# Performance work log

Measured on AMD Instinct MI355X. Metric: run time of the kernel, lower is better.

The kernel has to match this reference:

```python
import jax, jax.numpy as jnp
import numpy as np
from jax import lax

B, C, H, W = 8, 384, 64, 64


def cos_map(N):
    # ortho DCT-II basis: weight[n, x] = cos(n*(x+0.5)*pi/N) * sqrt(2/N), row 0 /= sqrt(2)
    wx = (jnp.arange(N, dtype=jnp.float32) + 0.5) / N
    wn = jnp.arange(N, dtype=jnp.float32)[:, None]
    w = jnp.cos(wn * wx[None, :] * jnp.pi) * np.sqrt(2.0 / N).astype(np.float32)
    return w.at[0, :].multiply(np.float32(1.0 / np.sqrt(2.0)))


def setup_inputs() -> dict:
    key = jax.random.key(0)
    ks = jax.random.split(key, 8)
    s = 0.05
    return {
        "x": jax.random.normal(ks[0], (B, C, H, W), jnp.float32),
        "freq_embed": jax.random.normal(ks[1], (H, W, C), jnp.float32),
        "dw_w": jax.random.normal(ks[2], (C, 1, 3, 3), jnp.float32) * s,
        "dw_b": jnp.zeros((C,), jnp.float32),
        "lin_w": jax.random.normal(ks[3], (2 * C, C), jnp.float32) * s,
        "lin_b": jnp.zeros((2 * C,), jnp.float32),
        "tok_w": jax.random.normal(ks[4], (C, C), jnp.float32) * s,
        "tok_b": jnp.zeros((C,), jnp.float32),
        "c": jnp.ones((1,), jnp.float32),
        "alpha": jnp.ones((1,), jnp.float32) * 0.1,
        "ln_g": jnp.ones((C,), jnp.float32),
        "ln_b": jnp.zeros((C,), jnp.float32),
        "out_w": jax.random.normal(ks[5], (C, C), jnp.float32) * s,
        "out_b": jnp.zeros((C,), jnp.float32),
    }


def reference(x, freq_embed, dw_w, dw_b, lin_w, lin_b, tok_w, tok_b, c, alpha, ln_g, ln_b, out_w, out_b):
    Bc, Cc, Hc, Wc = x.shape
    # depthwise 3x3 conv
    x = lax.conv_general_dilated(x, dw_w, (1, 1), 'SAME',
                                 feature_group_count=Cc,
                                 dimension_numbers=('NCHW', 'OIHW', 'NCHW'))
    x = x + dw_b[None, :, None, None]
    # linear to 2C (channels-last), split into signal x and gate z
    xz = jnp.einsum('bchw,dc->bhwd', x, lin_w) + lin_b
    xs, z = xz[..., :Cc], xz[..., Cc:]          # [B,H,W,C]
    xs = jnp.transpose(xs, (0, 3, 1, 2))        # [B,C,H,W]
    # 2D ortho DCT-II: D = Wh @ x @ Ww^T
    Wh, Ww = cos_map(Hc), cos_map(Wc)
    Xd = jnp.einsum('nh,bchw,kw->bcnk', Wh, xs, Ww)
    # learned frequency gating: t = ReLU(Linear(freq_embed)), per (H,W,C)
    t = jax.nn.relu(jnp.einsum('hwc,dc->hwd', freq_embed, tok_w) + tok_b)
    ct = jnp.transpose(jnp.cos(c * t), (2, 0, 1))[None]        # [1,C,H,W]
    st = jnp.transpose(jnp.sin(c * t), (2, 0, 1))[None] / c[0]
    # x_u0 == x_v0 == Xd in the original (dct2d applied twice to same x)
    final = ct * Xd + st * (Xd + 0.5 * alpha[0] * Xd)
    # 2D inverse DCT: x = Wh^T @ D @ Ww
    xi = jnp.einsum('nh,bcnk,kw->bchw', Wh, final, Ww)
    # LayerNorm over channels, gate with SiLU(z), output linear
    y = jnp.transpose(xi, (0, 2, 3, 1))          # [B,H,W,C]
    mu = jnp.mean(y, axis=-1, keepdims=True)
    var = jnp.mean((y - mu) ** 2, axis=-1, keepdims=True)
    y = (y - mu) * lax.rsqrt(var + 1e-5) * ln_g + ln_b
    y = y * jax.nn.silu(z)
    y = jnp.einsum('bhwc,dc->bhwd', y, out_w) + out_b
    return jnp.transpose(y, (0, 3, 1, 2))        # [B,C,H,W]
```

## Files before the change

kernel.cpp:

```cpp
#include <hip/hip_runtime.h>

typedef _Float16 h2 __attribute__((ext_vector_type(2)));
typedef _Float16 h4 __attribute__((ext_vector_type(4)));
typedef _Float16 h8 __attribute__((ext_vector_type(8)));
typedef float    f4 __attribute__((ext_vector_type(4)));

#define MFMA32(a,b,c) __builtin_amdgcn_mfma_f32_16x16x32_f16((a),(b),(c),0,0,0)
#define MFMA16(a,b,c) __builtin_amdgcn_mfma_f32_16x16x16f16((a),(b),(c),0,0,0)

#define B_N 8
#define C_N 384
#define P_N 4096
#define PI_F 3.14159265358979323846f

__device__ __forceinline__ h4 to_h4(f4 v) {
  h4 r; r[0]=(_Float16)v[0]; r[1]=(_Float16)v[1]; r[2]=(_Float16)v[2]; r[3]=(_Float16)v[3];
  return r;
}

__device__ __forceinline__ void gl_lds16(const _Float16* g, _Float16* l) {
  __builtin_amdgcn_global_load_lds(
      (const __attribute__((address_space(1))) void*)g,
      (__attribute__((address_space(3))) void*)l, 16, 0, 0);
}

__device__ __forceinline__ void gemm_step(
    const _Float16* __restrict__ ga, const _Float16* __restrict__ gb,
    int kcn, bool pref,
    _Float16* laC, _Float16* lbC, _Float16* laN, _Float16* lbN,
    f4 (&acc)[4][4]) {
  int t = threadIdx.x, lane = t & 63, wave = t >> 6;
  int quad = lane >> 4, l15 = lane & 15;
  int wm = wave >> 1, wn = wave & 1;
  int s_row = lane >> 2;
  if (pref) {
    #pragma unroll
    for (int s = 0; s < 2; s++) {
      int seg = wave * 2 + s;
      int row = seg * 16 + s_row;
      gl_lds16(ga + (size_t)row*384 + kcn, &laN[seg*512 + lane*8]);
      gl_lds16(gb + (size_t)row*384 + kcn, &lbN[seg*512 + lane*8]);
    }
    asm volatile("s_waitcnt vmcnt(4)" ::: "memory");
  } else {
    asm volatile("s_waitcnt vmcnt(0)" ::: "memory");
  }
  __builtin_amdgcn_s_barrier();
  asm volatile("" ::: "memory");
  h8 af[4], bf[4];
  int sq = (quad ^ (l15 & 3)) * 8;
  #pragma unroll
  for (int i = 0; i < 4; i++) {
    af[i] = *(const h8*)&laC[(wm*64 + i*16 + l15)*32 + sq];
    bf[i] = *(const h8*)&lbC[(wn*64 + i*16 + l15)*32 + sq];
  }
  asm volatile("s_waitcnt lgkmcnt(0)" ::: "memory");
  __builtin_amdgcn_s_barrier();
  asm volatile("" ::: "memory");
  #pragma unroll
  for (int i = 0; i < 4; i++)
  #pragma unroll
  for (int j = 0; j < 4; j++)
    acc[i][j] = MFMA32(af[i], bf[j], acc[i][j]);
}

__global__ __launch_bounds__(256) void k_setup(
    const float* __restrict__ lin_w, const float* __restrict__ tok_w,
    const float* __restrict__ out_w, _Float16* __restrict__ lwh,
    _Float16* __restrict__ twh, _Float16* __restrict__ owh,
    _Float16* __restrict__ wmg, _Float16* __restrict__ wmtg) {
  int t = blockIdx.x * 256 + threadIdx.x;
  if (t < 768*384) lwh[t] = (_Float16)lin_w[t];
  if (t < 384*384) { twh[t] = (_Float16)tok_w[t]; owh[t] = (_Float16)out_w[t]; }
  if (t < 4096) {
    int n = t >> 6, h = t & 63;
    float v = cosf((float)n * ((float)h + 0.5f) * (PI_F / 64.0f)) * 0.1767766952966369f;
    if (n == 0) v *= 0.7071067811865476f;
    wmg[n*64 + h]  = (_Float16)v;
    wmtg[h*64 + n] = (_Float16)v;
  }
}

__global__ __launch_bounds__(256) void k_dwconv(
    const float* __restrict__ x, const float* __restrict__ dww,
    const float* __restrict__ dwb, _Float16* __restrict__ xdw) {
  int blk = blockIdx.x;
  int h = blk & 63;
  int rest = blk >> 6;
  int cgi = rest % 6;
  int b = rest / 6;
  int c0 = cgi * 64;
  int t = threadIdx.x;
  __shared__ float wsm[576];
  __shared__ float bsm[64];
  __shared__ _Float16 buf[64 * 68];
  for (int i = t; i < 576; i += 256) wsm[i] = dww[c0*9 + i];
  if (t < 64) bsm[t] = dwb[c0 + t];
  __syncthreads();
  int lane = t & 63;
  int wslot = lane & 15, w4 = wslot * 4;
  int cs = t >> 4;
  bool wlo = (wslot == 0), whi = (wslot == 15);
  int lm = (lane - 1) & 63, lp = (lane + 1) & 63;
  const float* xb = x + (size_t)b * C_N * P_N;
  float pr[4][4];
  #pragma unroll
  for (int q = 0; q < 4; q++) {
    int lc = cs * 4 + q;
    const float* xc = xb + (size_t)(c0 + lc) * P_N + h * 64 + w4;
    f4 mid = *(const f4*)xc;
    f4 top = {}, bot = {};
    if (h > 0)  top = *(const f4*)(xc - 64);
    if (h < 63) bot = *(const f4*)(xc + 64);
    float tL = __shfl(top[3], lm, 64), tR = __shfl(top[0], lp, 64);
    float mL = __shfl(mid[3], lm, 64), mR = __shfl(mid[0], lp, 64);
    float bL = __shfl(bot[3], lm, 64), bR = __shfl(bot[0], lp, 64);
    if (wlo) { tL = 0.f; mL = 0.f; bL = 0.f; }
    if (whi) { tR = 0.f; mR = 0.f; bR = 0.f; }
    float k0=wsm[lc*9+0],k1=wsm[lc*9+1],k2=wsm[lc*9+2];
    float k3=wsm[lc*9+3],k4=wsm[lc*9+4],k5=wsm[lc*9+5];
    float k6=wsm[lc*9+6],k7=wsm[lc*9+7],k8=wsm[lc*9+8];
    float bias = bsm[lc];
    #pragma unroll
    for (int e = 0; e < 4; e++) {
      float tl = (e > 0) ? top[e-1] : tL;
      float tr = (e < 3) ? top[e+1] : tR;
      float ml = (e > 0) ? mid[e-1] : mL;
      float mr = (e < 3) ? mid[e+1] : mR;
      float bl = (e > 0) ? bot[e-1] : bL;
      float br = (e < 3) ? bot[e+1] : bR;
      float acc = bias;
      acc += k0*tl + k1*top[e] + k2*tr;
      acc += k3*ml + k4*mid[e] + k5*mr;
      acc += k6*bl + k7*bot[e] + k8*br;
      pr[q][e] = acc;
    }
  }
  #pragma unroll
  for (int e = 0; e < 4; e++) {
    h4 hv;
    #pragma unroll
    for (int q = 0; q < 4; q++) hv[q] = (_Float16)pr[q][e];
    *(h4*)&buf[(w4 + e) * 68 + cs * 4] = hv;
  }
  __syncthreads();
  _Float16* op = xdw + ((size_t)b*P_N + h*64) * C_N + c0;
  #pragma unroll
  for (int i = 0; i < 4; i++) {
    int flat = (t + 256*i) * 4;
    int pix = flat >> 6, cl = flat & 63;
    *(h4*)&op[(size_t)pix*C_N + cl] = *(const h4*)&buf[pix*68 + cl];
  }
}

__global__ __launch_bounds__(256) void k_gate(
    const float* __restrict__ fe, const _Float16* __restrict__ twh,
    const float* __restrict__ tkb, const float* __restrict__ cc,
    const float* __restrict__ aa, _Float16* __restrict__ g) {
  int pt = blockIdx.x & 63, dt = blockIdx.x >> 6;
  int p0 = pt*64, d0 = dt*64;
  int t = threadIdx.x, lane = t & 63, wave = t >> 6;
  int quad = lane >> 4, l15 = lane & 15;
  int wm_ = wave >> 1, wn = wave & 1;
  __shared__ _Float16 la[64*40], lb[64*40];
  int srow = t >> 2, scg = (t & 3) * 8;
  f4 acc[2][2] = {};
  for (int kc = 0; kc < 384; kc += 32) {
    const float* src = fe + (size_t)(p0 + srow)*384 + kc + scg;
    f4 v0 = *(const f4*)src;
    f4 v1 = *(const f4*)(src + 4);
    h8 hv;
    hv[0]=(_Float16)v0[0]; hv[1]=(_Float16)v0[1]; hv[2]=(_Float16)v0[2]; hv[3]=(_Float16)v0[3];
    hv[4]=(_Float16)v1[0]; hv[5]=(_Float16)v1[1]; hv[6]=(_Float16)v1[2]; hv[7]=(_Float16)v1[3];
    *(h8*)&la[srow*40 + scg] = hv;
    *(h8*)&lb[srow*40 + scg] = *(const h8*)&twh[(size_t)(d0 + srow)*384 + kc + scg];
    __syncthreads();
    h8 a0 = *(const h8*)&la[(wm_*32 + l15)*40 + quad*8];
    h8 a1 = *(const h8*)&la[(wm_*32 + 16 + l15)*40 + quad*8];
    h8 b0 = *(const h8*)&lb[(wn*32 + l15)*40 + quad*8];
    h8 b1 = *(const h8*)&lb[(wn*32 + 16 + l15)*40 + quad*8];
    acc[0][0] = MFMA32(a0, b0, acc[0][0]);
    acc[0][1] = MFMA32(a0, b1, acc[0][1]);
    acc[1][0] = MFMA32(a1, b0, acc[1][0]);
    acc[1][1] = MFMA32(a1, b1, acc[1][1]);
    __syncthreads();
  }
  float c0 = cc[0];
  float s1 = (1.0f + 0.5f*aa[0]) / c0;
  #pragma unroll
  for (int i = 0; i < 2; i++)
  #pragma unroll
  for (int j = 0; j < 2; j++) {
    int d  = d0 + wn*32 + j*16 + l15;
    int pl = wm_*32 + i*16 + quad*4;
    float bias = tkb[d];
    h4 hv;
    #pragma unroll
    for (int r = 0; r < 4; r++) {
      float tv = fmaxf(acc[i][j][r] + bias, 0.0f);
      hv[r] = (_Float16)(__cosf(c0*tv) + s1*__sinf(c0*tv));
    }
    *(h4*)&g[(size_t)d*P_N + p0 + pl] = hv;
  }
}

__global__ __launch_bounds__(256) void k_gemm1(
    const _Float16* __restrict__ xdw, const _Float16* __restrict__ lwh,
    const float* __restrict__ lnb, _Float16* __restrict__ xs,
    _Float16* __restrict__ zs) {
  int pt = blockIdx.x & 31;
  int rest = blockIdx.x >> 5;
  int dt = rest % 6, b = rest / 6;
  int p0 = pt * 128, d0 = dt * 128;
  int t = threadIdx.x, lane = t & 63, wave = t >> 6;
  int quad = lane >> 4, l15 = lane & 15;
  int wm = wave >> 1, wn = wave & 1;
  __shared__ _Float16 la0[128 * 32], lb0[128 * 32];
  __shared__ _Float16 la1[128 * 32], lb1[128 * 32];
  int s_row = lane >> 2;
  int scol2 = (((lane & 3) ^ (s_row & 3)) * 8);
  const _Float16* ga = xdw + ((size_t)b*P_N + p0) * 384 + scol2;
  const _Float16* gb = lwh + (size_t)d0 * 384 + scol2;
  f4 acc[4][4] = {};
  #pragma unroll
  for (int s = 0; s < 2; s++) {
    int seg = wave * 2 + s;
    int row = seg * 16 + s_row;
    gl_lds16(ga + (size_t)row*384, &la0[seg*512 + lane*8]);
    gl_lds16(gb + (size_t)row*384, &lb0[seg*512 + lane*8]);
  }
  #pragma unroll
  for (int kt = 0; kt < 6; kt++) {
    int kc = kt * 64;
    gemm_step(ga, gb, kc + 32,  true,            la0, lb0, la1, lb1, acc);
    gemm_step(ga, gb, kc + 64,  (kc + 64 < 384), la1, lb1, la0, lb0, acc);
  }
  bool isz = (d0 >= 384);
  #pragma unroll
  for (int j = 0; j < 4; j++) {
    int d = d0 + wn*64 + j*16 + l15;
    float bias = lnb[d];
    _Float16* dst = isz ? (zs + ((size_t)b*C_N + (d-384)) * P_N)
                        : (xs + ((size_t)b*C_N + d) * P_N);
    #pragma unroll
    for (int i = 0; i < 4; i++) {
      int p = p0 + wm*64 + i*16 + quad*4;
      h4 hv;
      if (isz) {
        #pragma unroll
        for (int r = 0; r < 4; r++) {
          float v = acc[i][j][r] + bias;
          v = v / (1.0f + __expf(-v));
          hv[r] = (_Float16)v;
        }
      } else {
        #pragma unroll
        for (int r = 0; r < 4; r++) hv[r] = (_Float16)(acc[i][j][r] + bias);
      }
      *(h4*)&dst[p] = hv;
    }
  }
}

__global__ __launch_bounds__(256) void k_dct(
    const _Float16* __restrict__ xs, const _Float16* __restrict__ g,
    const _Float16* __restrict__ wmg, const _Float16* __restrict__ wmtg,
    _Float16* __restrict__ xi) {
  int b = blockIdx.x / 96, cg = blockIdx.x % 96;
  int c0 = cg * 4;
  int t = threadIdx.x, wave = t >> 6, lane = t & 63;
  int quad = lane >> 4, l15 = lane & 15;
  __shared__ _Float16 wm_s[64*72];
  __shared__ _Float16 wmt_s[64*72];
  __shared__ _Float16 pb[4][64*72];
  for (int i = t; i < 512; i += 256) {
    int row = i >> 3, col = (i & 7) * 8;
    *(h8*)&wm_s[row*72 + col]  = *(const h8*)&wmg[row*64 + col];
    *(h8*)&wmt_s[row*72 + col] = *(const h8*)&wmtg[row*64 + col];
  }
  const _Float16* xsb = xs + ((size_t)b*C_N + c0) * P_N;
  for (int i = t; i < 2048; i += 256) {
    int pl = i >> 9, idx = i & 511;
    int p = idx * 8, hh = p >> 6, ww = p & 63;
    *(h8*)&pb[pl][hh*72 + ww] = *(const h8*)&xsb[(size_t)pl*P_N + p];
  }
  __syncthreads();
  h8 aS[4][2], bW[4][2];
  #pragma unroll
  for (int I = 0; I < 4; I++)
  #pragma unroll
  for (int kk = 0; kk < 2; kk++) {
    aS[I][kk] = *(const h8*)&pb[wave][(I*16 + l15)*72 + kk*32 + quad*8];
    bW[I][kk] = *(const h8*)&wm_s[(I*16 + l15)*72 + kk*32 + quad*8];
  }
  h4 t1h[4][4];
  #pragma unroll
  for (int I = 0; I < 4; I++)
  #pragma unroll
  for (int J = 0; J < 4; J++) {
    f4 a = {};
    a = MFMA32(aS[I][0], bW[J][0], a);
    a = MFMA32(aS[I][1], bW[J][1], a);
    t1h[I][J] = to_h4(a);
  }
  __syncthreads();
  const _Float16* gb = g + (size_t)c0 * P_N;
  for (int i = t; i < 2048; i += 256) {
    int pl = i >> 9, idx = i & 511;
    int p = idx * 8, hh = p >> 6, ww = p & 63;
    *(h8*)&pb[pl][hh*72 + ww] = *(const h8*)&gb[(size_t)pl*P_N + p];
  }
  __syncthreads();
  f4 t2[4][4] = {};
  #pragma unroll
  for (int I = 0; I < 4; I++)
  #pragma unroll
  for (int K4 = 0; K4 < 4; K4++) {
    h4 af = *(const h4*)&wm_s[(I*16 + l15)*72 + K4*16 + quad*4];
    #pragma unroll
    for (int J = 0; J < 4; J++) t2[I][J] = MFMA16(af, t1h[K4][J], t2[I][J]);
  }
  h4 fh[4][4];
  #pragma unroll
  for (int I = 0; I < 4; I++)
  #pragma unroll
  for (int J = 0; J < 4; J++) {
    int n0 = I*16 + quad*4, k = J*16 + l15;
    h4 r;
    #pragma unroll
    for (int rr = 0; rr < 4; rr++) {
      float gv = (float)pb[wave][(n0+rr)*72 + k];
      r[rr] = (_Float16)(t2[I][J][rr] * gv);
    }
    fh[I][J] = r;
  }
  f4 t3[4][4] = {};
  #pragma unroll
  for (int J = 0; J < 4; J++)
  #pragma unroll
  for (int K4 = 0; K4 < 4; K4++) {
    h4 bf = *(const h4*)&wmt_s[(J*16 + l15)*72 + K4*16 + quad*4];
    #pragma unroll
    for (int I = 0; I < 4; I++) t3[I][J] = MFMA16(fh[K4][I], bf, t3[I][J]);
  }
  h4 t3h[4][4];
  #pragma unroll
  for (int I = 0; I < 4; I++)
  #pragma unroll
  for (int J = 0; J < 4; J++) t3h[I][J] = to_h4(t3[I][J]);
  f4 t4[4][4] = {};
  #pragma unroll
  for (int I = 0; I < 4; I++)
  #pragma unroll
  for (int K4 = 0; K4 < 4; K4++) {
    h4 af = *(const h4*)&wmt_s[(I*16 + l15)*72 + K4*16 + quad*4];
    #pragma unroll
    for (int J = 0; J < 4; J++) t4[I][J] = MFMA16(af, t3h[K4][J], t4[I][J]);
  }
  #pragma unroll
  for (int I = 0; I < 4; I++)
  #pragma unroll
  for (int J = 0; J < 4; J++) {
    int w0 = I*16 + quad*4, hq = J*16 + l15;
    *(h4*)&pb[wave][hq*72 + w0] = to_h4(t4[I][J]);
  }
  __syncthreads();
  _Float16* xib = xi + ((size_t)b*C_N + c0) * P_N;
  for (int i = t; i < 2048; i += 256) {
    int pl = i >> 9, idx = i & 511;
    int p = idx * 8, hh = p >> 6, ww = p & 63;
    *(h8*)&xib[(size_t)pl*P_N + p] = *(const h8*)&pb[pl][hh*72 + ww];
  }
}

__global__ __launch_bounds__(256) void k_ubuild(
    const _Float16* __restrict__ xi, const _Float16* __restrict__ zs,
    const float* __restrict__ lng, const float* __restrict__ lnbv,
    _Float16* __restrict__ u) {
  int b = blockIdx.x >> 6, pt = blockIdx.x & 63;
  int p0 = pt * 64;
  int t = threadIdx.x;
  __shared__ _Float16 ut[64 * 392];
  __shared__ float red[4][64], red2[4][64];
  __shared__ float muL[64], rsL[64];
  const _Float16* xib = xi + (size_t)b * C_N * P_N;
  #pragma unroll
  for (int i = 0; i < 3; i++) {
    int id = t + 256 * i;
    int px0 = (id & 7) * 8;
    int c4 = (id >> 3) * 4;
    h8 v[4];
    #pragma unroll
    for (int q = 0; q < 4; q++)
      v[q] = *(const h8*)&xib[(size_t)(c4 + q) * P_N + p0 + px0];
    #pragma unroll
    for (int e = 0; e < 8; e++) {
      h4 w;
      #pragma unroll
      for (int q = 0; q < 4; q++) w[q] = v[q][e];
      *(h4*)&ut[(px0 + e) * 392 + c4] = w;
    }
  }
  __syncthreads();
  int px = t & 63, seg = t >> 6;
  float s = 0.f, ss = 0.f;
  #pragma unroll
  for (int j = 0; j < 12; j++) {
    h8 v = *(const h8*)&ut[px * 392 + seg * 96 + j * 8];
    #pragma unroll
    for (int e = 0; e < 8; e++) { float f = (float)v[e]; s += f; ss += f * f; }
  }
  red[seg][px] = s; red2[seg][px] = ss;
  __syncthreads();
  if (t < 64) {
    float st  = red[0][t] + red[1][t] + red[2][t] + red[3][t];
    float sst = red2[0][t] + red2[1][t] + red2[2][t] + red2[3][t];
    float m = st * (1.f/384.f);
    float var = sst * (1.f/384.f) - m * m;
    muL[t] = m; rsL[t] = rsqrtf(var + 1e-5f);
  }
  __syncthreads();
  const _Float16* zb = zs + (size_t)b * C_N * P_N;
  #pragma unroll
  for (int i = 0; i < 3; i++) {
    int id = t + 256 * i;
    int px0 = (id & 7) * 8;
    int c4 = (id >> 3) * 4;
    f4 g4 = *(const f4*)&lng[c4];
    f4 b4 = *(const f4*)&lnbv[c4];
    h8 z[4];
    #pragma unroll
    for (int q = 0; q < 4; q++)
      z[q] = *(const h8*)&zb[(size_t)(c4 + q) * P_N + p0 + px0];
    #pragma unroll
    for (int e = 0; e < 8; e++) {
      int p = px0 + e;
      h4 y = *(const h4*)&ut[p * 392 + c4];
      float mu = muL[p], rs = rsL[p];
      #pragma unroll
      for (int q = 0; q < 4; q++) {
        float f = ((float)y[q] - mu) * rs * g4[q] + b4[q];
        y[q] = (_Float16)(f * (float)z[q][e]);
      }
      *(h4*)&ut[p * 392 + c4] = y;
    }
  }
  __syncthreads();
  _Float16* ub = u + ((size_t)b * P_N + p0) * C_N;
  #pragma unroll
  for (int i = 0; i < 12; i++) {
    int idx = t + 256 * i;
    int row = idx / 48, ch = idx % 48;
    *(h8*)&ub[(size_t)row * C_N + ch * 8] = *(const h8*)&ut[row * 392 + ch * 8];
  }
}

__global__ __launch_bounds__(256) void k_gemm2(
    const _Float16* __restrict__ u, const _Float16* __restrict__ owh,
    const float* __restrict__ ob, float* __restrict__ out) {
  int pt = blockIdx.x & 31;
  int rest = blockIdx.x >> 5;
  int dt = rest % 3, b = rest / 3;
  int p0 = pt * 128, d0 = dt * 128;
  int t = threadIdx.x, lane = t & 63, wave = t >> 6;
  int quad = lane >> 4, l15 = lane & 15;
  int wm = wave >> 1, wn = wave & 1;
  __shared__ _Float16 la0[128 * 32], lb0[128 * 32];
  __shared__ _Float16 la1[128 * 32], lb1[128 * 32];
  int s_row = lane >> 2;
  int scol2 = (((lane & 3) ^ (s_row & 3)) * 8);
  const _Float16* ga = u   + ((size_t)b*P_N + p0) * 384 + scol2;
  const _Float16* gb = owh + (size_t)d0 * 384 + scol2;
  f4 acc[4][4] = {};
  #pragma unroll
  for (int s = 0; s < 2; s++) {
    int seg = wave * 2 + s;
    int row = seg * 16 + s_row;
    gl_lds16(ga + (size_t)row*384, &la0[seg*512 + lane*8]);
    gl_lds16(gb + (size_t)row*384, &lb0[seg*512 + lane*8]);
  }
  #pragma unroll
  for (int kt = 0; kt < 6; kt++) {
    int kc = kt * 64;
    gemm_step(ga, gb, kc + 32,  true,            la0, lb0, la1, lb1, acc);
    gemm_step(ga, gb, kc + 64,  (kc + 64 < 384), la1, lb1, la0, lb0, acc);
  }
  #pragma unroll
  for (int j = 0; j < 4; j++) {
    int d = d0 + wn*64 + j*16 + l15;
    float bias = ob[d];
    #pragma unroll
    for (int i = 0; i < 4; i++) {
      int p = p0 + wm*64 + i*16 + quad*4;
      f4 v;
      #pragma unroll
      for (int r = 0; r < 4; r++) v[r] = acc[i][j][r] + bias;
      *(f4*)&out[((size_t)b*C_N + d)*P_N + p] = v;
    }
  }
}

extern "C" void kernel_launch(void* const* d_in, const int* in_sizes, int n_in,
                              void* d_out, int out_size, void* d_ws, size_t ws_size,
                              hipStream_t stream) {
  (void)in_sizes; (void)n_in; (void)out_size; (void)ws_size;
  const float* x    = (const float*)d_in[0];
  const float* fe   = (const float*)d_in[1];
  const float* dww  = (const float*)d_in[2];
  const float* dwb  = (const float*)d_in[3];
  const float* linw = (const float*)d_in[4];
  const float* linb = (const float*)d_in[5];
  const float* tokw = (const float*)d_in[6];
  const float* tokb = (const float*)d_in[7];
  const float* cc   = (const float*)d_in[8];
  const float* aa   = (const float*)d_in[9];
  const float* lng  = (const float*)d_in[10];
  const float* lnbv = (const float*)d_in[11];
  const float* outw = (const float*)d_in[12];
  const float* outb = (const float*)d_in[13];
  float* out = (float*)d_out;

  char* ws = (char*)d_ws;
  size_t off = 0;
  auto alloc = [&](size_t bytes) -> void* {
    void* p = ws + off;
    off += (bytes + 255) & ~(size_t)255;
    return p;
  };
  _Float16* lwh  = (_Float16*)alloc((size_t)768*384*2);
  _Float16* twh  = (_Float16*)alloc((size_t)384*384*2);
  _Float16* owh  = (_Float16*)alloc((size_t)384*384*2);
  _Float16* wmg  = (_Float16*)alloc((size_t)64*64*2);
  _Float16* wmtg = (_Float16*)alloc((size_t)64*64*2);
  _Float16* xdw  = (_Float16*)alloc((size_t)B_N*P_N*C_N*2);
  _Float16* xs   = (_Float16*)alloc((size_t)B_N*C_N*P_N*2);
  _Float16* zs   = (_Float16*)alloc((size_t)B_N*C_N*P_N*2);
  _Float16* gg   = (_Float16*)alloc((size_t)C_N*P_N*2);
  _Float16* xi   = xdw;
  _Float16* uu   = xs;

  k_setup<<<1152, 256, 0, stream>>>(linw, tokw, outw, lwh, twh, owh, wmg, wmtg);
  k_dwconv<<<3072, 256, 0, stream>>>(x, dww, dwb, xdw);
  k_gate<<<384, 256, 0, stream>>>(fe, twh, tokb, cc, aa, gg);
  k_gemm1<<<1536, 256, 0, stream>>>(xdw, lwh, linb, xs, zs);
  k_dct<<<768, 256, 0, stream>>>(xs, gg, wmg, wmtg, xi);
  k_ubuild<<<512, 256, 0, stream>>>(xi, zs, lng, lnbv, uu);
  k_gemm2<<<768, 256, 0, stream>>>(uu, owh, outb, out);
}
```

Baseline: 234.7 us.

## Process four rows per dwconv block with rolling row reuse; transpose gate tile in LDS

The depthwise conv kernel now handles four consecutive rows per block and keeps the previous and current input rows in registers. Each input row is loaded about once instead of three times, and the grid shrinks fourfold. Separately, the DCT kernel now stores the gate tile transposed in LDS, so the gate multiply can read four contiguous halves per lane instead of four strided scalar loads. The cost is more registers and a larger LDS buffer in dwconv, plus fewer blocks to spread across the GPU.

```diff
diff --git a/kernel.cpp b/kernel.cpp
--- a/kernel.cpp
+++ b/kernel.cpp
@@ -85,15 +85,16 @@
     const float* __restrict__ x, const float* __restrict__ dww,
     const float* __restrict__ dwb, _Float16* __restrict__ xdw) {
   int blk = blockIdx.x;
-  int h = blk & 63;
-  int rest = blk >> 6;
+  int hs = blk & 15;
+  int rest = blk >> 4;
   int cgi = rest % 6;
   int b = rest / 6;
   int c0 = cgi * 64;
+  int h0 = hs * 4;
   int t = threadIdx.x;
   __shared__ float wsm[576];
   __shared__ float bsm[64];
-  __shared__ _Float16 buf[64 * 68];
+  __shared__ _Float16 buf[4][64 * 68];
   for (int i = t; i < 576; i += 256) wsm[i] = dww[c0*9 + i];
   if (t < 64) bsm[t] = dwb[c0 + t];
   __syncthreads();
@@ -102,54 +103,70 @@
   int cs = t >> 4;
   bool wlo = (wslot == 0), whi = (wslot == 15);
   int lm = (lane - 1) & 63, lp = (lane + 1) & 63;
-  const float* xb = x + (size_t)b * C_N * P_N;
-  float pr[4][4];
+  const float* xb = x + (size_t)b * C_N * P_N + w4;
+  f4 prev[4], cur[4];
+  float pL[4], pR[4], cL[4], cR[4];
   #pragma unroll
   for (int q = 0; q < 4; q++) {
-    int lc = cs * 4 + q;
-    const float* xc = xb + (size_t)(c0 + lc) * P_N + h * 64 + w4;
-    f4 mid = *(const f4*)xc;
-    f4 top = {}, bot = {};
-    if (h > 0)  top = *(const f4*)(xc - 64);
-    if (h < 63) bot = *(const f4*)(xc + 64);
-    float tL = __shfl(top[3], lm, 64), tR = __shfl(top[0], lp, 64);
-    float mL = __shfl(mid[3], lm, 64), mR = __shfl(mid[0], lp, 64);
-    float bL = __shfl(bot[3], lm, 64), bR = __shfl(bot[0], lp, 64);
-    if (wlo) { tL = 0.f; mL = 0.f; bL = 0.f; }
-    if (whi) { tR = 0.f; mR = 0.f; bR = 0.f; }
-    float k0=wsm[lc*9+0],k1=wsm[lc*9+1],k2=wsm[lc*9+2];
-    float k3=wsm[lc*9+3],k4=wsm[lc*9+4],k5=wsm[lc*9+5];
-    float k6=wsm[lc*9+6],k7=wsm[lc*9+7],k8=wsm[lc*9+8];
-    float bias = bsm[lc];
+    const float* xc = xb + (size_t)(c0 + cs*4 + q) * P_N;
+    prev[q] = (h0 > 0) ? *(const f4*)(xc + (h0-1)*64) : f4{0.f,0.f,0.f,0.f};
+    cur[q]  = *(const f4*)(xc + h0*64);
+    pL[q] = __shfl(prev[q][3], lm, 64); pR[q] = __shfl(prev[q][0], lp, 64);
+    cL[q] = __shfl(cur[q][3],  lm, 64); cR[q] = __shfl(cur[q][0],  lp, 64);
+    if (wlo) { pL[q] = 0.f; cL[q] = 0.f; }
+    if (whi) { pR[q] = 0.f; cR[q] = 0.f; }
+  }
+  #pragma unroll
+  for (int r = 0; r < 4; r++) {
+    int h = h0 + r;
+    float o[4][4];
+    #pragma unroll
+    for (int q = 0; q < 4; q++) {
+      int lc = cs*4 + q;
+      const float* xc = xb + (size_t)(c0 + lc) * P_N;
+      f4 nxt = (h < 63) ? *(const f4*)(xc + (h+1)*64) : f4{0.f,0.f,0.f,0.f};
+      float nL = __shfl(nxt[3], lm, 64), nR = __shfl(nxt[0], lp, 64);
+      if (wlo) nL = 0.f;
+      if (whi) nR = 0.f;
+      float k0=wsm[lc*9+0],k1=wsm[lc*9+1],k2=wsm[lc*9+2];
+      float k3=wsm[lc*9+3],k4=wsm[lc*9+4],k5=wsm[lc*9+5];
+      float k6=wsm[lc*9+6],k7=wsm[lc*9+7],k8=wsm[lc*9+8];
+      float bias = bsm[lc];
+      #pragma unroll
+      for (int e = 0; e < 4; e++) {
+        float tl = (e > 0) ? prev[q][e-1] : pL[q];
+        float tr = (e < 3) ? prev[q][e+1] : pR[q];
+        float ml = (e > 0) ? cur[q][e-1]  : cL[q];
+        float mr = (e < 3) ? cur[q][e+1]  : cR[q];
+        float bl = (e > 0) ? nxt[e-1]     : nL;
+        float br = (e < 3) ? nxt[e+1]     : nR;
+        float acc = bias;
+        acc += k0*tl + k1*prev[q][e] + k2*tr;
+        acc += k3*ml + k4*cur[q][e]  + k5*mr;
+        acc += k6*bl + k7*nxt[e]     + k8*br;
+        o[q][e] = acc;
+      }
+      prev[q] = cur[q]; pL[q] = cL[q]; pR[q] = cR[q];
+      cur[q] = nxt;     cL[q] = nL;    cR[q] = nR;
+    }
     #pragma unroll
     for (int e = 0; e < 4; e++) {
-      float tl = (e > 0) ? top[e-1] : tL;
-      float tr = (e < 3) ? top[e+1] : tR;
-      float ml = (e > 0) ? mid[e-1] : mL;
-      float mr = (e < 3) ? mid[e+1] : mR;
-      float bl = (e > 0) ? bot[e-1] : bL;
-      float br = (e < 3) ? bot[e+1] : bR;
-      float acc = bias;
-      acc += k0*tl + k1*top[e] + k2*tr;
-      acc += k3*ml + k4*mid[e] + k5*mr;
-      acc += k6*bl + k7*bot[e] + k8*br;
-      pr[q][e] = acc;
-    }
-  }
-  #pragma unroll
-  for (int e = 0; e < 4; e++) {
-    h4 hv;
-    #pragma unroll
-    for (int q = 0; q < 4; q++) hv[q] = (_Float16)pr[q][e];
-    *(h4*)&buf[(w4 + e) * 68 + cs * 4] = hv;
-  }
-  __syncthreads();
-  _Float16* op = xdw + ((size_t)b*P_N + h*64) * C_N + c0;
-  #pragma unroll
-  for (int i = 0; i < 4; i++) {
-    int flat = (t + 256*i) * 4;
-    int pix = flat >> 6, cl = flat & 63;
-    *(h4*)&op[(size_t)pix*C_N + cl] = *(const h4*)&buf[pix*68 + cl];
+      h4 hv;
+      #pragma unroll
+      for (int q = 0; q < 4; q++) hv[q] = (_Float16)o[q][e];
+      *(h4*)&buf[r][(w4 + e) * 68 + cs * 4] = hv;
+    }
+  }
+  __syncthreads();
+  #pragma unroll
+  for (int r = 0; r < 4; r++) {
+    _Float16* op = xdw + ((size_t)b*P_N + (h0 + r)*64) * C_N + c0;
+    #pragma unroll
+    for (int i = 0; i < 4; i++) {
+      int flat = (t + 256*i) * 4;
+      int pix = flat >> 6, cl = flat & 63;
+      *(h4*)&op[(size_t)pix*C_N + cl] = *(const h4*)&buf[r][pix*68 + cl];
+    }
   }
 }
 
@@ -305,10 +322,24 @@
   }
   __syncthreads();
   const _Float16* gb = g + (size_t)c0 * P_N;
-  for (int i = t; i < 2048; i += 256) {
-    int pl = i >> 9, idx = i & 511;
-    int p = idx * 8, hh = p >> 6, ww = p & 63;
-    *(h8*)&pb[pl][hh*72 + ww] = *(const h8*)&gb[(size_t)pl*P_N + p];
+  #pragma unroll
+  for (int i = 0; i < 2; i++) {
+    int id = t + 256 * i;
+    int pl = id >> 7;
+    int r7 = id & 127;
+    int n4 = (r7 >> 3) * 4;
+    int k8 = (r7 & 7) * 8;
+    h8 v[4];
+    #pragma unroll
+    for (int q = 0; q < 4; q++)
+      v[q] = *(const h8*)&gb[(size_t)pl*P_N + (n4 + q)*64 + k8];
+    #pragma unroll
+    for (int e = 0; e < 8; e++) {
+      h4 w;
+      #pragma unroll
+      for (int q = 0; q < 4; q++) w[q] = v[q][e];
+      *(h4*)&pb[pl][(k8 + e)*72 + n4] = w;
+    }
   }
   __syncthreads();
   f4 t2[4][4] = {};
@@ -325,13 +356,11 @@
   for (int I = 0; I < 4; I++)
   #pragma unroll
   for (int J = 0; J < 4; J++) {
-    int n0 = I*16 + quad*4, k = J*16 + l15;
+    h4 gv4 = *(const h4*)&pb[wave][(J*16 + l15)*72 + I*16 + quad*4];
     h4 r;
     #pragma unroll
-    for (int rr = 0; rr < 4; rr++) {
-      float gv = (float)pb[wave][(n0+rr)*72 + k];
-      r[rr] = (_Float16)(t2[I][J][rr] * gv);
-    }
+    for (int rr = 0; rr < 4; rr++)
+      r[rr] = (_Float16)(t2[I][J][rr] * (float)gv4[rr]);
     fh[I][J] = r;
   }
   f4 t3[4][4] = {};
@@ -540,7 +569,7 @@
   _Float16* uu   = xs;
 
   k_setup<<<1152, 256, 0, stream>>>(linw, tokw, outw, lwh, twh, owh, wmg, wmtg);
-  k_dwconv<<<3072, 256, 0, stream>>>(x, dww, dwb, xdw);
+  k_dwconv<<<768, 256, 0, stream>>>(x, dww, dwb, xdw);
   k_gate<<<384, 256, 0, stream>>>(fe, twh, tokb, cc, aa, gg);
   k_gemm1<<<1536, 256, 0, stream>>>(xdw, lwh, linb, xs, zs);
   k_dct<<<768, 256, 0, stream>>>(xs, gg, wmg, wmtg, xi);
```

New measurement: 232.9 us. No clear change (-0.8%).
